# Kernel tuning notes

Hardware: AMD Instinct MI355X
Metric: run time of the kernel (lower is better)

## Reference

```python
import jax, jax.numpy as jnp
import numpy as np

D_MODEL = 1024
N_HEAD = 16
DH = D_MODEL // N_HEAD


def setup_inputs() -> dict:
    key = jax.random.key(0)
    ks = jax.random.split(key, 5)
    B, T = 4, 2048
    scale = 0.02
    return {
        "x": jax.random.normal(ks[0], (B, T, D_MODEL), dtype=jnp.float32),
        "Wqkv": jax.random.normal(ks[1], (D_MODEL, 3 * D_MODEL), dtype=jnp.float32) * scale,
        "bqkv": jnp.zeros((3 * D_MODEL,), dtype=jnp.float32),
        "Wout": jax.random.normal(ks[2], (D_MODEL, D_MODEL), dtype=jnp.float32) * scale,
        "bout": jnp.zeros((D_MODEL,), dtype=jnp.float32),
    }


def reference(x, Wqkv, bqkv, Wout, bout):
    B, T, C = x.shape
    qkv = x @ Wqkv + bqkv  # [B,T,3C]
    q, k, v = jnp.split(qkv, 3, axis=2)
    # [B,T,C] -> [B,H,T,dh]
    def heads(t):
        return t.reshape(B, T, N_HEAD, DH).transpose(0, 2, 1, 3)
    q, k, v = heads(q), heads(k), heads(v)
    scores = jnp.einsum("bhqd,bhkd->bhqk", q, k) / jnp.sqrt(jnp.float32(DH))
    causal = jnp.tril(jnp.ones((T, T), dtype=bool))  # [T,T]
    neg = jnp.finfo(scores.dtype).min
    scores = jnp.where(causal[None, None, :, :], scores, neg)
    A = jax.nn.softmax(scores, axis=-1)
    y = jnp.einsum("bhqk,bhkd->bhqd", A, v)
    y = y.transpose(0, 2, 1, 3).reshape(B, T, C)
    return y @ Wout + bout
```

## Files before the change

kernel.cpp:

```cpp
#include <hip/hip_runtime.h>
#include <hip/hip_bf16.h>

typedef float f32x4 __attribute__((ext_vector_type(4)));
typedef float f32x16 __attribute__((ext_vector_type(16)));
typedef short s16x8 __attribute__((ext_vector_type(8)));
typedef short s16x4 __attribute__((ext_vector_type(4)));
typedef unsigned int u32x4 __attribute__((ext_vector_type(4)));

#define B_ 4
#define T_ 2048
#define C_ 1024
#define H_ 16
#define DH_ 64
#define M_ (B_*T_)
#define N3_ (3*C_)

static __device__ __forceinline__ short f2bf(float f) {
    __hip_bfloat16 h = __float2bfloat16(f);
    return *reinterpret_cast<short*>(&h);
}

static __device__ __forceinline__ unsigned pack2(float lo, float hi) {
    unsigned lb = (unsigned short)f2bf(lo);
    unsigned hb = (unsigned short)f2bf(hi);
    return lb | (hb << 16);
}

static __device__ __forceinline__ void gload16(const void* g, void* l) {
    __builtin_amdgcn_global_load_lds(
        (const __attribute__((address_space(1))) void*)g,
        (__attribute__((address_space(3))) void*)l, 16, 0, 0);
}

static __device__ __forceinline__ s16x8 lds_frag(const short* base, int row, int chunk) {
    return *(const s16x8*)&base[(row << 6) + ((chunk ^ (row & 7)) << 3)];
}

static __device__ __forceinline__ s16x8 vfrag(const short* base, int row, int kc, int h) {
    int r7 = row & 7;
    s16x4 a = *(const s16x4*)&base[(row << 6) + (((2 * kc) ^ r7) << 3) + 4 * h];
    s16x4 b = *(const s16x4*)&base[(row << 6) + (((2 * kc + 1) ^ r7) << 3) + 4 * h];
    return __builtin_shufflevector(a, b, 0, 1, 2, 3, 4, 5, 6, 7);
}


__global__ __launch_bounds__(256) void cast_f32_bf16(
    const float* __restrict__ in, short* __restrict__ out, int n8)
{
    int i = blockIdx.x * 256 + threadIdx.x;
    if (i >= n8) return;
    float4 a = *(const float4*)&in[i * 8];
    float4 b = *(const float4*)&in[i * 8 + 4];
    s16x8 o = { f2bf(a.x), f2bf(a.y), f2bf(a.z), f2bf(a.w),
                f2bf(b.x), f2bf(b.y), f2bf(b.z), f2bf(b.w) };
    *(s16x8*)&out[i * 8] = o;
}

__global__ __launch_bounds__(256) void transpose_cast(
    const float* __restrict__ src, short* __restrict__ dst, int K, int N)
{
    __shared__ short t[64][66];
    int tid = threadIdx.x;
    int n0 = blockIdx.x * 64, k0 = blockIdx.y * 64;
    #pragma unroll
    for (int p = 0; p < 4; ++p) {
        int cid = tid + p * 256;
        int r = cid >> 4, c4 = cid & 15;
        float4 v = *(const float4*)&src[(size_t)(k0 + r) * N + n0 + c4 * 4];
        t[r][c4 * 4 + 0] = f2bf(v.x);
        t[r][c4 * 4 + 1] = f2bf(v.y);
        t[r][c4 * 4 + 2] = f2bf(v.z);
        t[r][c4 * 4 + 3] = f2bf(v.w);
    }
    __syncthreads();
    #pragma unroll
    for (int p = 0; p < 4; ++p) {
        int cid = tid + p * 256;
        int r = cid >> 4, c4 = cid & 15;
        s16x4 ov;
        #pragma unroll
        for (int j = 0; j < 4; ++j) ov[j] = t[c4 * 4 + j][r];
        *(s16x4*)&dst[(size_t)(n0 + r) * K + k0 + c4 * 4] = ov;
    }
}


template<int MODE>
__global__ __launch_bounds__(256) void gemm_bt(
    const short* __restrict__ A, const short* __restrict__ Bt,
    const float* __restrict__ bias, float* __restrict__ out,
    short* __restrict__ qout, short* __restrict__ kout, short* __restrict__ vout)
{
    const int K = 1024;
    __shared__ short As[128 * 64];
    __shared__ short Bs[128 * 64];
    int tid = threadIdx.x;
    int lane = tid & 63, w = tid >> 6;
    int d = lane & 15, g = lane >> 4;
    int wm = w >> 1, wn = w & 1;
    int m0 = blockIdx.y * 128, n0 = blockIdx.x * 128;

    f32x4 acc[4][4];
    #pragma unroll
    for (int i = 0; i < 4; ++i)
        #pragma unroll
        for (int j = 0; j < 4; ++j) acc[i][j] = (f32x4){0.f, 0.f, 0.f, 0.f};

    for (int kt = 0; kt < K; kt += 64) {
        #pragma unroll
        for (int p = 0; p < 4; ++p) {
            int cid = p * 256 + tid;
            int r = cid >> 3, c8 = cid & 7;
            int co = (c8 ^ (r & 7)) << 3;
            int dofs = (p * 256 + (tid & ~63)) * 8;
            gload16(&A[(size_t)(m0 + r) * K + kt + co], &As[dofs]);
            gload16(&Bt[(size_t)(n0 + r) * K + kt + co], &Bs[dofs]);
        }
        __syncthreads();
        #pragma unroll
        for (int ks = 0; ks < 2; ++ks) {
            s16x8 af[4], bf[4];
            #pragma unroll
            for (int i = 0; i < 4; ++i) {
                af[i] = lds_frag(As, wm * 64 + i * 16 + d, ks * 4 + g);
                bf[i] = lds_frag(Bs, wn * 64 + i * 16 + d, ks * 4 + g);
            }
            #pragma unroll
            for (int mi = 0; mi < 4; ++mi)
                #pragma unroll
                for (int ni = 0; ni < 4; ++ni)
                    acc[mi][ni] = __builtin_amdgcn_mfma_f32_16x16x32_bf16(
                        af[mi], bf[ni], acc[mi][ni], 0, 0, 0);
        }
        __syncthreads();
    }

    #pragma unroll
    for (int mi = 0; mi < 4; ++mi)
        #pragma unroll
        for (int ni = 0; ni < 4; ++ni) {
            int gn = n0 + wn * 64 + ni * 16 + d;
            float bv = bias[gn];
            int gm0 = m0 + wm * 64 + mi * 16 + g * 4;
            if (MODE == 0) {
                #pragma unroll
                for (int r = 0; r < 4; ++r)
                    out[(size_t)(gm0 + r) * 1024 + gn] = acc[mi][ni][r] + bv;
            } else {
                int which = gn >> 10, cc = gn & 1023;
                int h = cc >> 6, dh = cc & 63;
                int b = gm0 >> 11, t0 = gm0 & 2047;
                if (which == 2) {
                    s16x4 pv;
                    #pragma unroll
                    for (int r = 0; r < 4; ++r) pv[r] = f2bf(acc[mi][ni][r] + bv);
                    *(s16x4*)&vout[((size_t)(b * 16 + h) * 64 + dh) * 2048 + t0] = pv;
                } else if (which == 1) {
                    #pragma unroll
                    for (int r = 0; r < 4; ++r)
                        kout[((size_t)(b * 16 + h) * 2048 + (t0 + r)) * 64 + dh] =
                            f2bf(acc[mi][ni][r] + bv);
                } else {
                    const float SC2 = 0.125f * 1.44269504089f;
                    #pragma unroll
                    for (int r = 0; r < 4; ++r)
                        qout[((size_t)(b * 16 + h) * 2048 + (t0 + r)) * 64 + dh] =
                            f2bf((acc[mi][ni][r] + bv) * SC2);
                }
            }
        }
}


__global__ __launch_bounds__(256, 4) void attn_fwd(
    const short* __restrict__ q, const short* __restrict__ kk,
    const short* __restrict__ vt, short* __restrict__ y)
{
    __shared__ short Ks[2][64 * 64];
    __shared__ short Vs[2][64 * 64];
    int tid = threadIdx.x, w = tid >> 6;
    int lane = tid & 63;
    int q5 = lane & 31, h5 = lane >> 5;
    int bid = blockIdx.x;
    int idx = bid >> 3;
    int qt = 15 - (idx >> 3);
    int bh = ((idx & 7) << 3) | (bid & 7);
    int b = bh >> 4, hh = bh & 15;
    const size_t hb = (size_t)bh * 2048 * 64;
    int nt = 2 * qt + 2;
    int qrow = qt * 128 + w * 32;
    int qg = qrow + q5;

    s16x8 qf[4];
    #pragma unroll
    for (int s = 0; s < 4; ++s)
        qf[s] = *(const s16x8*)&q[hb + (size_t)qg * 64 + 16 * s + 8 * h5];

    f32x16 oA, oB;
    #pragma unroll
    for (int i = 0; i < 16; ++i) { oA[i] = 0.f; oB[i] = 0.f; }
    float l = 0.f;

    #define STAGE(buf, kt2) do { \
        _Pragma("unroll") \
        for (int p = 0; p < 2; ++p) { \
            int cid = p * 256 + tid; \
            int r__ = cid >> 3, c8__ = cid & 7; \
            int co__ = (c8__ ^ (r__ & 7)) << 3; \
            int dofs__ = (p * 256 + (tid & ~63)) * 8; \
            gload16(&kk[hb + (size_t)((kt2) * 64 + r__) * 64 + co__], &Ks[buf][dofs__]); \
            gload16(&vt[hb + (size_t)r__ * 2048 + (kt2) * 64 + co__], &Vs[buf][dofs__]); \
        } \
    } while (0)

    STAGE(0, 0);
    int cur = 0;

    #pragma unroll 1
    for (int t = 0; t < nt; ++t) {
        if (t + 1 < nt) {
            STAGE(cur ^ 1, t + 1);
            asm volatile("s_waitcnt vmcnt(4)" ::: "memory");
        } else {
            asm volatile("s_waitcnt vmcnt(0)" ::: "memory");
        }
        __builtin_amdgcn_s_barrier();

        if (t * 64 <= qrow + 31) {
            const short* Kb = Ks[cur];
            const short* Vb = Vs[cur];

            f32x16 sA, sB;
            #pragma unroll
            for (int i = 0; i < 16; ++i) { sA[i] = 0.f; sB[i] = 0.f; }
            #pragma unroll
            for (int s = 0; s < 4; ++s) {
                sA = __builtin_amdgcn_mfma_f32_32x32x16_bf16(
                    lds_frag(Kb, q5, 2 * s + h5), qf[s], sA, 0, 0, 0);
                sB = __builtin_amdgcn_mfma_f32_32x32x16_bf16(
                    lds_frag(Kb, 32 + q5, 2 * s + h5), qf[s], sB, 0, 0, 0);
            }

            float eA[16], eB[16];
            float S = 0.f;
            if (t * 64 + 63 > qrow) {
                #pragma unroll
                for (int rg = 0; rg < 16; ++rg) {
                    int kg = t * 64 + (rg & 3) + 8 * (rg >> 2) + 4 * h5;
                    float a = exp2f(sA[rg]); if (kg > qg) a = 0.f;
                    float c = exp2f(sB[rg]); if (kg + 32 > qg) c = 0.f;
                    eA[rg] = a; eB[rg] = c; S += a + c;
                }
            } else {
                #pragma unroll
                for (int rg = 0; rg < 16; ++rg) {
                    float a = exp2f(sA[rg]);
                    float c = exp2f(sB[rg]);
                    eA[rg] = a; eB[rg] = c; S += a + c;
                }
            }
            l += S;

            unsigned wdA[8], wdB[8];
            #pragma unroll
            for (int m = 0; m < 4; ++m) {
                wdA[2 * m]     = pack2(eA[4 * m],     eA[4 * m + 1]);
                wdA[2 * m + 1] = pack2(eA[4 * m + 2], eA[4 * m + 3]);
                wdB[2 * m]     = pack2(eB[4 * m],     eB[4 * m + 1]);
                wdB[2 * m + 1] = pack2(eB[4 * m + 2], eB[4 * m + 3]);
            }

            #pragma unroll
            for (int kc = 0; kc < 2; ++kc) {
                u32x4 pw = {wdA[4 * kc], wdA[4 * kc + 1], wdA[4 * kc + 2], wdA[4 * kc + 3]};
                s16x8 pb = __builtin_bit_cast(s16x8, pw);
                oA = __builtin_amdgcn_mfma_f32_32x32x16_bf16(
                    vfrag(Vb, q5, kc, h5), pb, oA, 0, 0, 0);
                oB = __builtin_amdgcn_mfma_f32_32x32x16_bf16(
                    vfrag(Vb, 32 + q5, kc, h5), pb, oB, 0, 0, 0);
            }
            #pragma unroll
            for (int kc = 0; kc < 2; ++kc) {
                u32x4 pw = {wdB[4 * kc], wdB[4 * kc + 1], wdB[4 * kc + 2], wdB[4 * kc + 3]};
                s16x8 pb = __builtin_bit_cast(s16x8, pw);
                oA = __builtin_amdgcn_mfma_f32_32x32x16_bf16(
                    vfrag(Vb, q5, kc + 2, h5), pb, oA, 0, 0, 0);
                oB = __builtin_amdgcn_mfma_f32_32x32x16_bf16(
                    vfrag(Vb, 32 + q5, kc + 2, h5), pb, oB, 0, 0, 0);
            }
        }

        __builtin_amdgcn_s_barrier();
        cur ^= 1;
    }

    l += __shfl_xor(l, 32);
    float rl = 1.0f / l;

    short* yp = &y[(size_t)(b * 2048 + qg) * 1024 + hh * 64];
    #pragma unroll
    for (int m = 0; m < 4; ++m) {
        s16x4 v0, v1;
        #pragma unroll
        for (int i = 0; i < 4; ++i) {
            v0[i] = f2bf(oA[4 * m + i] * rl);
            v1[i] = f2bf(oB[4 * m + i] * rl);
        }
        *(s16x4*)&yp[8 * m + 4 * h5] = v0;
        *(s16x4*)&yp[32 + 8 * m + 4 * h5] = v1;
    }
    #undef STAGE
}


extern "C" void kernel_launch(void* const* d_in, const int* in_sizes, int n_in,
                              void* d_out, int out_size, void* d_ws, size_t ws_size,
                              hipStream_t stream)
{
    const float* x    = (const float*)d_in[0];
    const float* Wqkv = (const float*)d_in[1];
    const float* bqkv = (const float*)d_in[2];
    const float* Wout = (const float*)d_in[3];
    const float* bout = (const float*)d_in[4];
    float* out = (float*)d_out;

    char* ws = (char*)d_ws;
    short* xbf   = (short*)ws;  ws += (size_t)M_ * C_ * 2;
    short* wqkvT = (short*)ws;  ws += (size_t)N3_ * C_ * 2;
    short* woutT = (short*)ws;  ws += (size_t)C_ * C_ * 2;
    short* qb    = (short*)ws;  ws += (size_t)M_ * C_ * 2;
    short* kb    = (short*)ws;  ws += (size_t)M_ * C_ * 2;
    short* vtb   = (short*)ws;  ws += (size_t)M_ * C_ * 2;
    short* yb    = (short*)ws;  ws += (size_t)M_ * C_ * 2;

    cast_f32_bf16<<<(M_ * C_ / 8 + 255) / 256, 256, 0, stream>>>(x, xbf, M_ * C_ / 8);
    transpose_cast<<<dim3(N3_ / 64, C_ / 64), 256, 0, stream>>>(Wqkv, wqkvT, C_, N3_);
    transpose_cast<<<dim3(C_ / 64, C_ / 64), 256, 0, stream>>>(Wout, woutT, C_, C_);

    gemm_bt<1><<<dim3(N3_ / 128, M_ / 128), 256, 0, stream>>>(
        xbf, wqkvT, bqkv, nullptr, qb, kb, vtb);

    attn_fwd<<<dim3((T_ / 128) * B_ * H_), 256, 0, stream>>>(qb, kb, vtb, yb);

    gemm_bt<0><<<dim3(C_ / 128, M_ / 128), 256, 0, stream>>>(
        yb, woutT, bout, out, nullptr, nullptr, nullptr);
}
```

Before: 185.9 us.

## Permute V layout for single-load fragments, pack bf16 via asm, swizzle GEMM blocks

The QKV GEMM epilogue now writes V^T with the 4-token groups permuted, so each attention V fragment becomes one 16-byte LDS read instead of two 8-byte reads plus a shuffle. P packing now uses the v_cvt_pk_bf16_f32 instruction in place of two scalar conversions. GEMM block IDs are remapped into 8 interleaved chunks, likely to improve cache locality across XCDs. The V permutation must match the attention kernel's MFMA k-ordering exactly, otherwise the output is wrong.

```diff
diff --git a/kernel.cpp b/kernel.cpp
--- a/kernel.cpp
+++ b/kernel.cpp
@@ -21,9 +21,9 @@
 }
 
 static __device__ __forceinline__ unsigned pack2(float lo, float hi) {
-    unsigned lb = (unsigned short)f2bf(lo);
-    unsigned hb = (unsigned short)f2bf(hi);
-    return lb | (hb << 16);
+    unsigned r;
+    asm("v_cvt_pk_bf16_f32 %0, %1, %2" : "=v"(r) : "v"(lo), "v"(hi));
+    return r;
 }
 
 static __device__ __forceinline__ void gload16(const void* g, void* l) {
@@ -34,13 +34,6 @@
 
 static __device__ __forceinline__ s16x8 lds_frag(const short* base, int row, int chunk) {
     return *(const s16x8*)&base[(row << 6) + ((chunk ^ (row & 7)) << 3)];
-}
-
-static __device__ __forceinline__ s16x8 vfrag(const short* base, int row, int kc, int h) {
-    int r7 = row & 7;
-    s16x4 a = *(const s16x4*)&base[(row << 6) + (((2 * kc) ^ r7) << 3) + 4 * h];
-    s16x4 b = *(const s16x4*)&base[(row << 6) + (((2 * kc + 1) ^ r7) << 3) + 4 * h];
-    return __builtin_shufflevector(a, b, 0, 1, 2, 3, 4, 5, 6, 7);
 }
 
 
@@ -98,7 +91,12 @@
     int lane = tid & 63, w = tid >> 6;
     int d = lane & 15, g = lane >> 4;
     int wm = w >> 1, wn = w & 1;
-    int m0 = blockIdx.y * 128, n0 = blockIdx.x * 128;
+
+    int gx = gridDim.x;
+    int lid = blockIdx.y * gx + blockIdx.x;
+    int chunk = (gx * gridDim.y) >> 3;
+    int sl = (lid & 7) * chunk + (lid >> 3);
+    int m0 = (sl / gx) * 128, n0 = (sl % gx) * 128;
 
     f32x4 acc[4][4];
     #pragma unroll
@@ -149,18 +147,22 @@
             } else {
                 int which = gn >> 10, cc = gn & 1023;
                 int h = cc >> 6, dh = cc & 63;
-                int b = gm0 >> 11, t0 = gm0 & 2047;
+                int b = gm0 >> 11;
                 if (which == 2) {
+                    int g2 = ((g & 1) << 1) | (g >> 1);
+                    int t0v = (gm0 & 2047) - g * 4 + g2 * 4;
                     s16x4 pv;
                     #pragma unroll
                     for (int r = 0; r < 4; ++r) pv[r] = f2bf(acc[mi][ni][r] + bv);
-                    *(s16x4*)&vout[((size_t)(b * 16 + h) * 64 + dh) * 2048 + t0] = pv;
+                    *(s16x4*)&vout[((size_t)(b * 16 + h) * 64 + dh) * 2048 + t0v] = pv;
                 } else if (which == 1) {
+                    int t0 = gm0 & 2047;
                     #pragma unroll
                     for (int r = 0; r < 4; ++r)
                         kout[((size_t)(b * 16 + h) * 2048 + (t0 + r)) * 64 + dh] =
                             f2bf(acc[mi][ni][r] + bv);
                 } else {
+                    int t0 = gm0 & 2047;
                     const float SC2 = 0.125f * 1.44269504089f;
                     #pragma unroll
                     for (int r = 0; r < 4; ++r)
@@ -271,22 +273,15 @@
             }
 
             #pragma unroll
-            for (int kc = 0; kc < 2; ++kc) {
-                u32x4 pw = {wdA[4 * kc], wdA[4 * kc + 1], wdA[4 * kc + 2], wdA[4 * kc + 3]};
+            for (int kc = 0; kc < 4; ++kc) {
+                const unsigned* wsrc = (kc < 2) ? wdA : wdB;
+                int o4 = (kc & 1) << 2;
+                u32x4 pw = {wsrc[o4], wsrc[o4 + 1], wsrc[o4 + 2], wsrc[o4 + 3]};
                 s16x8 pb = __builtin_bit_cast(s16x8, pw);
                 oA = __builtin_amdgcn_mfma_f32_32x32x16_bf16(
-                    vfrag(Vb, q5, kc, h5), pb, oA, 0, 0, 0);
+                    lds_frag(Vb, q5, 2 * kc + h5), pb, oA, 0, 0, 0);
                 oB = __builtin_amdgcn_mfma_f32_32x32x16_bf16(
-                    vfrag(Vb, 32 + q5, kc, h5), pb, oB, 0, 0, 0);
-            }
-            #pragma unroll
-            for (int kc = 0; kc < 2; ++kc) {
-                u32x4 pw = {wdB[4 * kc], wdB[4 * kc + 1], wdB[4 * kc + 2], wdB[4 * kc + 3]};
-                s16x8 pb = __builtin_bit_cast(s16x8, pw);
-                oA = __builtin_amdgcn_mfma_f32_32x32x16_bf16(
-                    vfrag(Vb, q5, kc + 2, h5), pb, oA, 0, 0, 0);
-                oB = __builtin_amdgcn_mfma_f32_32x32x16_bf16(
-                    vfrag(Vb, 32 + q5, kc + 2, h5), pb, oB, 0, 0, 0);
+                    lds_frag(Vb, 32 + q5, 2 * kc + h5), pb, oB, 0, 0, 0);
             }
         }
 
```

Result: no change. 182.5 us (-1.8%).
